# Performance work log

Measured on AMD Instinct MI355X. Metric: run time of the kernel, lower is better.

Reference implementation:

```python
import jax, jax.numpy as jnp
import numpy as np

N, E, D, H, C = 50000, 800000, 128, 1, 128  # nodes, edges, in_dim, heads, hidden
NEG_SLOPE = 0.2


def setup_inputs() -> dict:
    key = jax.random.key(0)
    ks = jax.random.split(key, 12)
    x = jax.random.normal(ks[0], (N, D), dtype=jnp.float32)
    edge_index = jax.random.randint(ks[1], (2, E), 0, N, dtype=jnp.int64)
    s = 1.0 / np.sqrt(D)
    inp = {"x": x, "edge_index": edge_index}
    for i, base in [(1, 2), (2, 7)]:
        inp[f"W{i}"] = jax.random.normal(ks[base], (D, H * C), dtype=jnp.float32) * s
        inp[f"att_src{i}"] = jax.random.normal(ks[base + 1], (H, C), dtype=jnp.float32) * s
        inp[f"att_dst{i}"] = jax.random.normal(ks[base + 2], (H, C), dtype=jnp.float32) * s
        inp[f"b{i}"] = jnp.zeros((C,), dtype=jnp.float32)
    return inp


def _gat_layer(x, src, dst, W, att_src, att_dst, b):
    n = x.shape[0]
    xl = (x @ W).reshape(n, H, C)                      # [N,H,C]
    a_s = jnp.sum(xl * att_src, axis=-1)               # [N,H]
    a_d = jnp.sum(xl * att_dst, axis=-1)               # [N,H]
    e = jax.nn.leaky_relu(a_s[src] + a_d[dst], NEG_SLOPE)  # [E',H]
    # segment softmax over incoming edges of each dst node
    m = jax.ops.segment_max(e, dst, num_segments=n)
    e = jnp.exp(e - m[dst])
    z = jax.ops.segment_sum(e, dst, num_segments=n)
    alpha = e / (z[dst] + 1e-16)                       # [E',H]
    msg = xl[src] * alpha[:, :, None]                  # [E',H,C]
    out = jax.ops.segment_sum(msg, dst, num_segments=n)  # [N,H,C]
    return out.mean(axis=1) + b                        # concat=False -> head mean


def reference(x, edge_index, W1, att_src1, att_dst1, b1, W2, att_src2, att_dst2, b2):
    # PyG GATConv default add_self_loops=True
    loops = jnp.arange(N, dtype=edge_index.dtype)
    src = jnp.concatenate([edge_index[0], loops])
    dst = jnp.concatenate([edge_index[1], loops])
    h = _gat_layer(x, src, dst, W1, att_src1, att_dst1, b1)
    h = jax.nn.relu(h)
    h = _gat_layer(h, src, dst, W2, att_src2, att_dst2, b2)
    return jax.nn.relu(h)
```

## Files before the change

### kernel.cpp

```cpp
#include <hip/hip_runtime.h>
#include <hip/hip_bf16.h>
#include <math.h>

#define NEG_SLOPE 0.2f

__device__ __forceinline__ float lrelu(float v) {
    return v > 0.0f ? v : NEG_SLOPE * v;
}

__device__ __forceinline__ float wred_sum(float v) {
    #pragma unroll
    for (int d = 32; d; d >>= 1) v += __shfl_xor(v, d);
    return v;
}

__device__ __forceinline__ unsigned short f2bf(float f) {
    unsigned u = __float_as_uint(f);
    return (unsigned short)((u + 0x7FFFu + ((u >> 16) & 1u)) >> 16);
}

__device__ __forceinline__ void bf8_fma(float* acc, uint4 u, float w) {
    acc[0] += w * __uint_as_float(u.x << 16);
    acc[1] += w * __uint_as_float(u.x & 0xFFFF0000u);
    acc[2] += w * __uint_as_float(u.y << 16);
    acc[3] += w * __uint_as_float(u.y & 0xFFFF0000u);
    acc[4] += w * __uint_as_float(u.z << 16);
    acc[5] += w * __uint_as_float(u.z & 0xFFFF0000u);
    acc[6] += w * __uint_as_float(u.w << 16);
    acc[7] += w * __uint_as_float(u.w & 0xFFFF0000u);
}

__global__ void k_zero4(int* __restrict__ p, int n4) {
    int i = blockIdx.x * blockDim.x + threadIdx.x;
    if (i < n4) ((int4*)p)[i] = make_int4(0, 0, 0, 0);
}

__global__ void k_hist_rank(const int* __restrict__ dst, int E,
                            int* __restrict__ counts, int* __restrict__ rank) {
    int i = blockIdx.x * blockDim.x + threadIdx.x;
    int base = i << 2;
    if (base + 3 < E) {
        int4 d = ((const int4*)dst)[i];
        int4 r;
        r.x = atomicAdd(&counts[d.x], 1);
        r.y = atomicAdd(&counts[d.y], 1);
        r.z = atomicAdd(&counts[d.z], 1);
        r.w = atomicAdd(&counts[d.w], 1);
        ((int4*)rank)[i] = r;
    } else {
        for (int j = base; j < E; ++j) rank[j] = atomicAdd(&counts[dst[j]], 1);
    }
}

__global__ void k_hist_rank_s(const int* __restrict__ dst, int E,
                              int* __restrict__ counts, int* __restrict__ rank) {
    int i = blockIdx.x * blockDim.x + threadIdx.x;
    if (i < E) rank[i] = atomicAdd(&counts[dst[i]], 1);
}

__global__ __launch_bounds__(1024) void k_scan(const int* __restrict__ counts,
                                               int* __restrict__ offsets, int n) {
    __shared__ int wsums[16];
    __shared__ int carry_sh;
    int tid = threadIdx.x;
    int lane = tid & 63;
    int wv = tid >> 6;
    if (tid == 0) carry_sh = 0;
    __syncthreads();
    int n4 = (n + 3) >> 2;
    for (int base = 0; base < n4; base += 1024) {
        int i = base + tid;
        int e0 = i << 2;
        int v0 = 0, v1 = 0, v2 = 0, v3 = 0;
        if (e0 + 3 < n) {
            int4 c = ((const int4*)counts)[i];
            v0 = c.x; v1 = c.y; v2 = c.z; v3 = c.w;
        } else if (e0 < n) {
            v0 = counts[e0];
            if (e0 + 1 < n) v1 = counts[e0 + 1];
            if (e0 + 2 < n) v2 = counts[e0 + 2];
        }
        int p1 = v0, p2 = p1 + v1, p3 = p2 + v2, tot = p3 + v3;
        int x = tot;
        #pragma unroll
        for (int d = 1; d < 64; d <<= 1) {
            int y = __shfl_up(x, d);
            if (lane >= d) x += y;
        }
        if (lane == 63) wsums[wv] = x;
        __syncthreads();
        if (wv == 0) {
            int s = (lane < 16) ? wsums[lane] : 0;
            #pragma unroll
            for (int d = 1; d < 16; d <<= 1) {
                int y = __shfl_up(s, d);
                if (lane >= d) s += y;
            }
            if (lane < 16) wsums[lane] = s;
        }
        __syncthreads();
        int excl = carry_sh + (wv > 0 ? wsums[wv - 1] : 0) + (x - tot);
        if (e0 + 3 < n) {
            ((int4*)offsets)[i] = make_int4(excl, excl + p1, excl + p2, excl + p3);
        } else if (e0 < n) {
            offsets[e0] = excl;
            if (e0 + 1 < n) offsets[e0 + 1] = excl + p1;
            if (e0 + 2 < n) offsets[e0 + 2] = excl + p2;
        }
        __syncthreads();
        if (tid == 0) carry_sh += wsums[15];
        __syncthreads();
    }
    if (tid == 0) offsets[n] = carry_sh;
}

__global__ void k_scatter(const int* __restrict__ src, const int* __restrict__ dst,
                          const int* __restrict__ rank, const int* __restrict__ offsets,
                          int E, int* __restrict__ csr_src) {
    int i = blockIdx.x * blockDim.x + threadIdx.x;
    int base = i << 2;
    if (base + 3 < E) {
        int4 s = ((const int4*)src)[i];
        int4 d = ((const int4*)dst)[i];
        int4 r = ((const int4*)rank)[i];
        csr_src[offsets[d.x] + r.x] = s.x;
        csr_src[offsets[d.y] + r.y] = s.y;
        csr_src[offsets[d.z] + r.z] = s.z;
        csr_src[offsets[d.w] + r.w] = s.w;
    } else {
        for (int j = base; j < E; ++j) csr_src[offsets[dst[j]] + rank[j]] = src[j];
    }
}

__global__ void k_scatter_s(const int* __restrict__ src, const int* __restrict__ dst,
                            const int* __restrict__ rank, const int* __restrict__ offsets,
                            int E, int* __restrict__ csr_src) {
    int i = blockIdx.x * blockDim.x + threadIdx.x;
    if (i < E) csr_src[offsets[dst[i]] + rank[i]] = src[i];
}

__global__ __launch_bounds__(256) void k_gemm_attn(const float* __restrict__ X,
                                                   const float* __restrict__ W,
                                                   const float* __restrict__ att_s,
                                                   const float* __restrict__ att_d,
                                                   unsigned short* __restrict__ XLb,
                                                   float* __restrict__ a_s,
                                                   float* __restrict__ a_d, int n) {
    __shared__ float XT[64 * 128];
    __shared__ float Wl[64 * 128];
    int tid = threadIdx.x;
    int row0 = blockIdx.x * 128;
    int c = tid & 15;
    int rg = tid >> 4;

    float acc[8][8] = {};
    for (int kb = 0; kb < 128; kb += 64) {
        __syncthreads();
        {
            const float4* W4 = (const float4*)(W + (size_t)kb * 128);
            float4* Wl4 = (float4*)Wl;
            #pragma unroll
            for (int i = 0; i < 8; ++i) Wl4[tid + i * 256] = W4[tid + i * 256];
        }
        {
            #pragma unroll
            for (int it = 0; it < 8; ++it) {
                int idx = tid + it * 256;
                int r = idx >> 4;
                int kq = idx & 15;
                int gr = row0 + r;
                float4 v = (gr < n) ? ((const float4*)X)[(size_t)gr * 32 + (kb >> 2) + kq]
                                    : make_float4(0.f, 0.f, 0.f, 0.f);
                int rs = r ^ ((kq & 7) << 2);
                float* dstp = &XT[(kq * 4) * 128 + rs];
                dstp[0 * 128] = v.x;
                dstp[1 * 128] = v.y;
                dstp[2 * 128] = v.z;
                dstp[3 * 128] = v.w;
            }
        }
        __syncthreads();
        #pragma unroll 2
        for (int kk = 0; kk < 64; ++kk) {
            int sw = ((kk >> 2) & 7) << 2;
            const float* xt = &XT[kk * 128];
            float4 xa = *(const float4*)&xt[(rg * 8) ^ sw];
            float4 xb = *(const float4*)&xt[(rg * 8 + 4) ^ sw];
            const float* wr = &Wl[kk * 128];
            float4 wa = *(const float4*)&wr[c * 4];
            float4 wb = *(const float4*)&wr[64 + c * 4];
            float xv[8] = {xa.x, xa.y, xa.z, xa.w, xb.x, xb.y, xb.z, xb.w};
            float wv[8] = {wa.x, wa.y, wa.z, wa.w, wb.x, wb.y, wb.z, wb.w};
            #pragma unroll
            for (int i = 0; i < 8; ++i)
                #pragma unroll
                for (int j = 0; j < 8; ++j)
                    acc[i][j] += xv[i] * wv[j];
        }
    }

    float4 as_a = ((const float4*)att_s)[c];
    float4 as_b = ((const float4*)att_s)[16 + c];
    float4 ad_a = ((const float4*)att_d)[c];
    float4 ad_b = ((const float4*)att_d)[16 + c];
    float asv[8] = {as_a.x, as_a.y, as_a.z, as_a.w, as_b.x, as_b.y, as_b.z, as_b.w};
    float adv[8] = {ad_a.x, ad_a.y, ad_a.z, ad_a.w, ad_b.x, ad_b.y, ad_b.z, ad_b.w};
    #pragma unroll
    for (int i = 0; i < 8; ++i) {
        float ps = 0.f, pd = 0.f;
        #pragma unroll
        for (int j = 0; j < 8; ++j) { ps += acc[i][j] * asv[j]; pd += acc[i][j] * adv[j]; }
        #pragma unroll
        for (int d = 1; d < 16; d <<= 1) { ps += __shfl_xor(ps, d); pd += __shfl_xor(pd, d); }
        int r = row0 + rg * 8 + i;
        if (c == 0 && r < n) { a_s[r] = ps; a_d[r] = pd; }
    }
    #pragma unroll
    for (int i = 0; i < 8; ++i) {
        int r = row0 + rg * 8 + i;
        if (r < n) {
            unsigned p0 = ((unsigned)f2bf(acc[i][1]) << 16) | f2bf(acc[i][0]);
            unsigned p1 = ((unsigned)f2bf(acc[i][3]) << 16) | f2bf(acc[i][2]);
            unsigned p2 = ((unsigned)f2bf(acc[i][5]) << 16) | f2bf(acc[i][4]);
            unsigned p3 = ((unsigned)f2bf(acc[i][7]) << 16) | f2bf(acc[i][6]);
            uint2* o = (uint2*)(XLb + (size_t)r * 128);
            o[c] = make_uint2(p0, p1);
            o[16 + c] = make_uint2(p2, p3);
        }
    }
}

__global__ __launch_bounds__(256) void k_aggregate(const unsigned short* __restrict__ xlb,
                                                   const float* __restrict__ a_s,
                                                   const float* __restrict__ a_d,
                                                   const int* __restrict__ csr_src,
                                                   const int* __restrict__ offsets,
                                                   const float* __restrict__ bias,
                                                   float* __restrict__ out, int n) {
    int wid = (blockIdx.x * blockDim.x + threadIdx.x) >> 6;
    int lane = threadIdx.x & 63;
    if (wid >= n) return;
    int beg = offsets[wid];
    int deg = offsets[wid + 1] - beg;
    float a_dn = a_d[wid];
    float w_self = __expf(lrelu(a_s[wid] + a_dn));

    int s_l = 0;
    float w_l = 0.0f;
    if (lane < deg) {
        s_l = csr_src[beg + lane];
        w_l = __expf(lrelu(a_s[s_l] + a_dn));
    }
    float zl = w_l;
    for (int j = 64 + lane; j < deg; j += 64) {
        int s = csr_src[beg + j];
        zl += __expf(lrelu(a_s[s] + a_dn));
    }
    float z = wred_sum(zl) + w_self;
    float inv = 1.0f / (z + 1e-16f);

    int qw = lane >> 4, ql = lane & 15;
    const uint4* xb4 = (const uint4*)xlb;
    float acc[8] = {};
    if (qw == 0) {
        uint4 u = xb4[(size_t)wid * 16 + ql];
        bf8_fma(acc, u, w_self);
    }
    int jmax = deg < 64 ? deg : 64;
    int nt = (jmax + 7) >> 3;
    for (int t = 0; t < nt; ++t) {
        int ja = (t << 3) + qw;
        int jb = ja + 4;
        int jca = ja < jmax ? ja : 0;
        int jcb = jb < jmax ? jb : 0;
        float wa = __shfl(w_l, jca);
        int sa = __shfl(s_l, jca);
        float wb = __shfl(w_l, jcb);
        int sb = __shfl(s_l, jcb);
        if (ja >= jmax) wa = 0.0f;
        if (jb >= jmax) wb = 0.0f;
        uint4 ua = xb4[(size_t)sa * 16 + ql];
        uint4 ub = xb4[(size_t)sb * 16 + ql];
        bf8_fma(acc, ua, wa);
        bf8_fma(acc, ub, wb);
    }
    for (int j = 64 + qw; j < deg; j += 4) {
        int sj = csr_src[beg + j];
        float wj = __expf(lrelu(a_s[sj] + a_dn));
        uint4 u = xb4[(size_t)sj * 16 + ql];
        bf8_fma(acc, u, wj);
    }
    #pragma unroll
    for (int k = 0; k < 8; ++k) {
        acc[k] += __shfl_xor(acc[k], 16);
        acc[k] += __shfl_xor(acc[k], 32);
    }
    if (qw == 0) {
        float4 b0 = ((const float4*)bias)[ql * 2];
        float4 b1 = ((const float4*)bias)[ql * 2 + 1];
        float4 r0, r1;
        r0.x = fmaxf(acc[0] * inv + b0.x, 0.0f);
        r0.y = fmaxf(acc[1] * inv + b0.y, 0.0f);
        r0.z = fmaxf(acc[2] * inv + b0.z, 0.0f);
        r0.w = fmaxf(acc[3] * inv + b0.w, 0.0f);
        r1.x = fmaxf(acc[4] * inv + b1.x, 0.0f);
        r1.y = fmaxf(acc[5] * inv + b1.y, 0.0f);
        r1.z = fmaxf(acc[6] * inv + b1.z, 0.0f);
        r1.w = fmaxf(acc[7] * inv + b1.w, 0.0f);
        ((float4*)out)[(size_t)wid * 32 + ql * 2] = r0;
        ((float4*)out)[(size_t)wid * 32 + ql * 2 + 1] = r1;
    }
}

extern "C" void kernel_launch(void* const* d_in, const int* in_sizes, int n_in,
                              void* d_out, int out_size, void* d_ws, size_t ws_size,
                              hipStream_t stream) {
    const float* x = (const float*)d_in[0];
    const int* edges = (const int*)d_in[1];
    const float* W1 = (const float*)d_in[2];
    const float* att_s1 = (const float*)d_in[3];
    const float* att_d1 = (const float*)d_in[4];
    const float* b1 = (const float*)d_in[5];
    const float* W2 = (const float*)d_in[6];
    const float* att_s2 = (const float*)d_in[7];
    const float* att_d2 = (const float*)d_in[8];
    const float* b2 = (const float*)d_in[9];

    const int N = in_sizes[0] / 128;
    const int E = in_sizes[1] / 2;
    const int* e_src = edges;
    const int* e_dst = edges + E;

    char* w = (char*)d_ws;
    auto carve = [&](size_t bytes) {
        char* p = w;
        w += (bytes + 255) & ~(size_t)255;
        return p;
    };
    const int n4 = (N + 3) >> 2;
    int* counts = (int*)carve((size_t)n4 * 16);
    int* offsets = (int*)carve((size_t)(N + 8) * 4);
    int* rank = (int*)carve((size_t)E * 4);
    int* csr_src = (int*)carve((size_t)E * 4);
    float* a_s = (float*)carve((size_t)N * 4);
    float* a_d = (float*)carve((size_t)N * 4);
    unsigned short* xlb = (unsigned short*)carve((size_t)N * 128 * 2);
    float* h = (float*)carve((size_t)N * 128 * 4);

    float* out = (float*)d_out;

    k_zero4<<<(n4 + 255) / 256, 256, 0, stream>>>(counts, n4);
    bool vec_ok = ((E & 3) == 0) && ((((uintptr_t)e_dst) & 15) == 0) &&
                  ((((uintptr_t)e_src) & 15) == 0);
    if (vec_ok) {
        int qb = (E / 4 + 255) / 256;
        k_hist_rank<<<qb, 256, 0, stream>>>(e_dst, E, counts, rank);
        k_scan<<<1, 1024, 0, stream>>>(counts, offsets, N);
        k_scatter<<<qb, 256, 0, stream>>>(e_src, e_dst, rank, offsets, E, csr_src);
    } else {
        int sb = (E + 255) / 256;
        k_hist_rank_s<<<sb, 256, 0, stream>>>(e_dst, E, counts, rank);
        k_scan<<<1, 1024, 0, stream>>>(counts, offsets, N);
        k_scatter_s<<<sb, 256, 0, stream>>>(e_src, e_dst, rank, offsets, E, csr_src);
    }

    int gemm_blocks = (N + 127) / 128;
    int wave_blocks = (N * 64 + 255) / 256;

    k_gemm_attn<<<gemm_blocks, 256, 0, stream>>>(x, W1, att_s1, att_d1, xlb, a_s, a_d, N);
    k_aggregate<<<wave_blocks, 256, 0, stream>>>(xlb, a_s, a_d, csr_src, offsets, b1, h, N);

    k_gemm_attn<<<gemm_blocks, 256, 0, stream>>>(h, W2, att_s2, att_d2, xlb, a_s, a_d, N);
    k_aggregate<<<wave_blocks, 256, 0, stream>>>(xlb, a_s, a_d, csr_src, offsets, b2, out, N);
}
```

Before: 216.3 us.

## Run projection GEMM on MFMA with split-bf16 three-pass emulation of fp32

Replaces the FP32 SIMT GEMM in the projection+attention kernel with bf16 MFMA 16x16x32 instructions. Inputs and weights are split into high and low bf16 parts and combined with three MFMAs to approximate FP32 accuracy. A new small kernel pre-splits and transposes W1/W2 into bf16 pairs each call. The attention-logit reduction is reworked to fit the MFMA output layout through shared memory. The extra split work and LDS traffic offset part of the matrix-core gain.

```diff
diff --git a/kernel.cpp b/kernel.cpp
--- a/kernel.cpp
+++ b/kernel.cpp
@@ -3,6 +3,9 @@
 #include <math.h>
 
 #define NEG_SLOPE 0.2f
+
+using bf16x8 = __attribute__((ext_vector_type(8))) short;
+using f32x4 = __attribute__((ext_vector_type(4))) float;
 
 __device__ __forceinline__ float lrelu(float v) {
     return v > 0.0f ? v : NEG_SLOPE * v;
@@ -139,93 +142,158 @@
     if (i < E) csr_src[offsets[dst[i]] + rank[i]] = src[i];
 }
 
+__global__ void k_wsplit(const float* __restrict__ W1, const float* __restrict__ W2,
+                         unsigned short* __restrict__ h1, unsigned short* __restrict__ l1,
+                         unsigned short* __restrict__ h2, unsigned short* __restrict__ l2) {
+    int i = blockIdx.x * blockDim.x + threadIdx.x;
+    int sel = i >> 14;
+    int j = i & 16383;
+    int nn = j >> 7, kk = j & 127;
+    const float* W = sel ? W2 : W1;
+    float f = W[kk * 128 + nn];
+    unsigned short h = f2bf(f);
+    float hf = __uint_as_float((unsigned)h << 16);
+    unsigned short lo = f2bf(f - hf);
+    if (sel) { h2[j] = h; l2[j] = lo; }
+    else     { h1[j] = h; l1[j] = lo; }
+}
+
 __global__ __launch_bounds__(256) void k_gemm_attn(const float* __restrict__ X,
-                                                   const float* __restrict__ W,
+                                                   const unsigned short* __restrict__ Wth,
+                                                   const unsigned short* __restrict__ Wtl,
                                                    const float* __restrict__ att_s,
                                                    const float* __restrict__ att_d,
                                                    unsigned short* __restrict__ XLb,
                                                    float* __restrict__ a_s,
                                                    float* __restrict__ a_d, int n) {
-    __shared__ float XT[64 * 128];
-    __shared__ float Wl[64 * 128];
-    int tid = threadIdx.x;
-    int row0 = blockIdx.x * 128;
-    int c = tid & 15;
-    int rg = tid >> 4;
-
-    float acc[8][8] = {};
+    __shared__ unsigned short WhT[8192];
+    __shared__ unsigned short WlT[8192];
+    __shared__ unsigned short XhT[8192];
+    __shared__ unsigned short XlT[8192];
+    __shared__ float pS[2][128];
+    __shared__ float pD[2][128];
+
+    const int tid = threadIdx.x;
+    const int row0 = blockIdx.x * 128;
+    const int wave = tid >> 6;
+    const int l = tid & 63;
+    const int lr = l & 15;
+    const int lg = l >> 4;
+    const int qm = (wave & 1) * 64;
+    const int qn = (wave >> 1) * 64;
+    const unsigned swz = (unsigned)(l & 7) << 4;
+
+    f32x4 acc[4][4];
+    #pragma unroll
+    for (int a = 0; a < 4; ++a)
+        #pragma unroll
+        for (int b = 0; b < 4; ++b)
+            acc[a][b] = (f32x4){0.f, 0.f, 0.f, 0.f};
+
     for (int kb = 0; kb < 128; kb += 64) {
         __syncthreads();
-        {
-            const float4* W4 = (const float4*)(W + (size_t)kb * 128);
-            float4* Wl4 = (float4*)Wl;
+        #pragma unroll
+        for (int it = 0; it < 4; ++it) {
+            int idx = it * 256 + tid;
+            int m = idx >> 3;
+            int kc = idx & 7;
+            int gr = row0 + m;
+            float4 v0 = make_float4(0.f, 0.f, 0.f, 0.f), v1 = v0;
+            if (gr < n) {
+                const float4* Xp = (const float4*)X + (size_t)gr * 32 + (kb >> 2) + (kc << 1);
+                v0 = Xp[0];
+                v1 = Xp[1];
+            }
+            float fv[8] = {v0.x, v0.y, v0.z, v0.w, v1.x, v1.y, v1.z, v1.w};
+            unsigned hp[4], lp[4];
             #pragma unroll
-            for (int i = 0; i < 8; ++i) Wl4[tid + i * 256] = W4[tid + i * 256];
-        }
-        {
+            for (int e = 0; e < 4; ++e) {
+                unsigned short h0 = f2bf(fv[2 * e]);
+                unsigned short h1 = f2bf(fv[2 * e + 1]);
+                float r0 = fv[2 * e] - __uint_as_float((unsigned)h0 << 16);
+                float r1 = fv[2 * e + 1] - __uint_as_float((unsigned)h1 << 16);
+                hp[e] = (unsigned)h0 | ((unsigned)h1 << 16);
+                lp[e] = (unsigned)f2bf(r0) | ((unsigned)f2bf(r1) << 16);
+            }
+            unsigned off = ((unsigned)m << 7) + ((unsigned)kc << 4);
+            unsigned so = off ^ (((unsigned)m & 7) << 4);
+            *(uint4*)((char*)XhT + so) = make_uint4(hp[0], hp[1], hp[2], hp[3]);
+            *(uint4*)((char*)XlT + so) = make_uint4(lp[0], lp[1], lp[2], lp[3]);
+            size_t wsrc = (size_t)m * 128 + kb + (kc << 3);
+            *(uint4*)((char*)WhT + so) = *(const uint4*)(Wth + wsrc);
+            *(uint4*)((char*)WlT + so) = *(const uint4*)(Wtl + wsrc);
+        }
+        __syncthreads();
+        #pragma unroll
+        for (int ks = 0; ks < 64; ks += 32) {
+            bf16x8 ah[4], al[4];
             #pragma unroll
-            for (int it = 0; it < 8; ++it) {
-                int idx = tid + it * 256;
-                int r = idx >> 4;
-                int kq = idx & 15;
-                int gr = row0 + r;
-                float4 v = (gr < n) ? ((const float4*)X)[(size_t)gr * 32 + (kb >> 2) + kq]
-                                    : make_float4(0.f, 0.f, 0.f, 0.f);
-                int rs = r ^ ((kq & 7) << 2);
-                float* dstp = &XT[(kq * 4) * 128 + rs];
-                dstp[0 * 128] = v.x;
-                dstp[1 * 128] = v.y;
-                dstp[2 * 128] = v.z;
-                dstp[3 * 128] = v.w;
-            }
-        }
-        __syncthreads();
-        #pragma unroll 2
-        for (int kk = 0; kk < 64; ++kk) {
-            int sw = ((kk >> 2) & 7) << 2;
-            const float* xt = &XT[kk * 128];
-            float4 xa = *(const float4*)&xt[(rg * 8) ^ sw];
-            float4 xb = *(const float4*)&xt[(rg * 8 + 4) ^ sw];
-            const float* wr = &Wl[kk * 128];
-            float4 wa = *(const float4*)&wr[c * 4];
-            float4 wb = *(const float4*)&wr[64 + c * 4];
-            float xv[8] = {xa.x, xa.y, xa.z, xa.w, xb.x, xb.y, xb.z, xb.w};
-            float wv[8] = {wa.x, wa.y, wa.z, wa.w, wb.x, wb.y, wb.z, wb.w};
+            for (int mt = 0; mt < 4; ++mt) {
+                unsigned ao = (((unsigned)(qm + mt * 16 + lr)) << 7) +
+                              ((unsigned)ks << 1) + ((unsigned)lg << 4);
+                ao ^= swz;
+                ah[mt] = *(const bf16x8*)((const char*)WhT + ao);
+                al[mt] = *(const bf16x8*)((const char*)WlT + ao);
+            }
             #pragma unroll
-            for (int i = 0; i < 8; ++i)
+            for (int nt = 0; nt < 4; ++nt) {
+                unsigned bo = (((unsigned)(qn + nt * 16 + lr)) << 7) +
+                              ((unsigned)ks << 1) + ((unsigned)lg << 4);
+                bo ^= swz;
+                bf16x8 bh = *(const bf16x8*)((const char*)XhT + bo);
+                bf16x8 bl = *(const bf16x8*)((const char*)XlT + bo);
                 #pragma unroll
-                for (int j = 0; j < 8; ++j)
-                    acc[i][j] += xv[i] * wv[j];
-        }
-    }
-
-    float4 as_a = ((const float4*)att_s)[c];
-    float4 as_b = ((const float4*)att_s)[16 + c];
-    float4 ad_a = ((const float4*)att_d)[c];
-    float4 ad_b = ((const float4*)att_d)[16 + c];
-    float asv[8] = {as_a.x, as_a.y, as_a.z, as_a.w, as_b.x, as_b.y, as_b.z, as_b.w};
-    float adv[8] = {ad_a.x, ad_a.y, ad_a.z, ad_a.w, ad_b.x, ad_b.y, ad_b.z, ad_b.w};
-    #pragma unroll
-    for (int i = 0; i < 8; ++i) {
+                for (int mt = 0; mt < 4; ++mt) {
+                    acc[mt][nt] = __builtin_amdgcn_mfma_f32_16x16x32_bf16(ah[mt], bh, acc[mt][nt], 0, 0, 0);
+                    acc[mt][nt] = __builtin_amdgcn_mfma_f32_16x16x32_bf16(al[mt], bh, acc[mt][nt], 0, 0, 0);
+                    acc[mt][nt] = __builtin_amdgcn_mfma_f32_16x16x32_bf16(ah[mt], bl, acc[mt][nt], 0, 0, 0);
+                }
+            }
+        }
+    }
+
+    float4 asv[4], adv[4];
+    #pragma unroll
+    for (int mt = 0; mt < 4; ++mt) {
+        asv[mt] = *(const float4*)&att_s[qm + mt * 16 + (lg << 2)];
+        adv[mt] = *(const float4*)&att_d[qm + mt * 16 + (lg << 2)];
+    }
+    #pragma unroll
+    for (int nt = 0; nt < 4; ++nt) {
         float ps = 0.f, pd = 0.f;
         #pragma unroll
-        for (int j = 0; j < 8; ++j) { ps += acc[i][j] * asv[j]; pd += acc[i][j] * adv[j]; }
-        #pragma unroll
-        for (int d = 1; d < 16; d <<= 1) { ps += __shfl_xor(ps, d); pd += __shfl_xor(pd, d); }
-        int r = row0 + rg * 8 + i;
-        if (c == 0 && r < n) { a_s[r] = ps; a_d[r] = pd; }
-    }
-    #pragma unroll
-    for (int i = 0; i < 8; ++i) {
-        int r = row0 + rg * 8 + i;
-        if (r < n) {
-            unsigned p0 = ((unsigned)f2bf(acc[i][1]) << 16) | f2bf(acc[i][0]);
-            unsigned p1 = ((unsigned)f2bf(acc[i][3]) << 16) | f2bf(acc[i][2]);
-            unsigned p2 = ((unsigned)f2bf(acc[i][5]) << 16) | f2bf(acc[i][4]);
-            unsigned p3 = ((unsigned)f2bf(acc[i][7]) << 16) | f2bf(acc[i][6]);
-            uint2* o = (uint2*)(XLb + (size_t)r * 128);
-            o[c] = make_uint2(p0, p1);
-            o[16 + c] = make_uint2(p2, p3);
+        for (int mt = 0; mt < 4; ++mt) {
+            f32x4 a = acc[mt][nt];
+            ps += a[0] * asv[mt].x + a[1] * asv[mt].y + a[2] * asv[mt].z + a[3] * asv[mt].w;
+            pd += a[0] * adv[mt].x + a[1] * adv[mt].y + a[2] * adv[mt].z + a[3] * adv[mt].w;
+        }
+        ps += __shfl_xor(ps, 16); ps += __shfl_xor(ps, 32);
+        pd += __shfl_xor(pd, 16); pd += __shfl_xor(pd, 32);
+        if (l < 16) {
+            pS[wave & 1][qn + nt * 16 + l] = ps;
+            pD[wave & 1][qn + nt * 16 + l] = pd;
+        }
+    }
+    #pragma unroll
+    for (int nt = 0; nt < 4; ++nt) {
+        int grow = row0 + qn + nt * 16 + lr;
+        if (grow < n) {
+            #pragma unroll
+            for (int mt = 0; mt < 4; ++mt) {
+                int col = qm + mt * 16 + (lg << 2);
+                f32x4 a = acc[mt][nt];
+                unsigned p0 = ((unsigned)f2bf(a[1]) << 16) | f2bf(a[0]);
+                unsigned p1 = ((unsigned)f2bf(a[3]) << 16) | f2bf(a[2]);
+                *(uint2*)(XLb + (size_t)grow * 128 + col) = make_uint2(p0, p1);
+            }
+        }
+    }
+    __syncthreads();
+    if (tid < 128) {
+        int gr = row0 + tid;
+        if (gr < n) {
+            a_s[gr] = pS[0][tid] + pS[1][tid];
+            a_d[gr] = pD[0][tid] + pD[1][tid];
         }
     }
 }
@@ -346,8 +414,14 @@
     float* a_d = (float*)carve((size_t)N * 4);
     unsigned short* xlb = (unsigned short*)carve((size_t)N * 128 * 2);
     float* h = (float*)carve((size_t)N * 128 * 4);
+    unsigned short* wth1 = (unsigned short*)carve(16384 * 2);
+    unsigned short* wtl1 = (unsigned short*)carve(16384 * 2);
+    unsigned short* wth2 = (unsigned short*)carve(16384 * 2);
+    unsigned short* wtl2 = (unsigned short*)carve(16384 * 2);
 
     float* out = (float*)d_out;
+
+    k_wsplit<<<128, 256, 0, stream>>>(W1, W2, wth1, wtl1, wth2, wtl2);
 
     k_zero4<<<(n4 + 255) / 256, 256, 0, stream>>>(counts, n4);
     bool vec_ok = ((E & 3) == 0) && ((((uintptr_t)e_dst) & 15) == 0) &&
@@ -367,9 +441,9 @@
     int gemm_blocks = (N + 127) / 128;
     int wave_blocks = (N * 64 + 255) / 256;
 
-    k_gemm_attn<<<gemm_blocks, 256, 0, stream>>>(x, W1, att_s1, att_d1, xlb, a_s, a_d, N);
+    k_gemm_attn<<<gemm_blocks, 256, 0, stream>>>(x, wth1, wtl1, att_s1, att_d1, xlb, a_s, a_d, N);
     k_aggregate<<<wave_blocks, 256, 0, stream>>>(xlb, a_s, a_d, csr_src, offsets, b1, h, N);
 
-    k_gemm_attn<<<gemm_blocks, 256, 0, stream>>>(h, W2, att_s2, att_d2, xlb, a_s, a_d, N);
+    k_gemm_attn<<<gemm_blocks, 256, 0, stream>>>(h, wth2, wtl2, att_s2, att_d2, xlb, a_s, a_d, N);
     k_aggregate<<<wave_blocks, 256, 0, stream>>>(xlb, a_s, a_d, csr_src, offsets, b2, out, N);
 }
```

New measurement: 181.2 us. 16.2% less time.
